# Optimization experiments

Measured on AMD Instinct MI355X. Metric: run time of the kernel, lower is better.

The kernel has to match this reference:

```python
import jax, jax.numpy as jnp
import numpy as np


def setup_inputs() -> dict:
    key = jax.random.key(0)
    ks = jax.random.split(key, 5)
    b, f, h, w, c = 2, 16, 64, 64, 256
    heads, D = 8, 32
    hD = heads * D
    x = jax.random.normal(ks[0], (b, f, h, w, c), dtype=jnp.float32)
    s = 1.0 / np.sqrt(c)
    Wq = jax.random.normal(ks[1], (c, hD), dtype=jnp.float32) * s
    Wk = jax.random.normal(ks[2], (c, hD), dtype=jnp.float32) * s
    Wv = jax.random.normal(ks[3], (c, hD), dtype=jnp.float32) * s
    Wo = jax.random.normal(ks[4], (hD, c), dtype=jnp.float32) * s
    return {"x": x, "Wq": Wq, "Wk": Wk, "Wv": Wv, "Wo": Wo, "heads": heads}


def reference(x, Wq, Wk, Wv, Wo, heads):
    b, f, h, w, c = x.shape
    hD = Wq.shape[1]
    D = hD // heads
    n = h * w
    # fuse batch & frames; 1x1 conv == channel matmul
    xf = x.reshape(b * f, n, c)  # [(bf), n, c]

    def proj(W):
        # [(bf), n, hD] -> [(bf), heads, D, n]
        p = jnp.einsum('bnc,cd->bnd', xf, W)
        return p.reshape(b * f, n, heads, D).transpose(0, 2, 3, 1)

    q = jax.nn.softmax(proj(Wq), axis=-2)  # softmax over D (note: scale is dead code in source)
    k = jax.nn.softmax(proj(Wk), axis=-1)  # softmax over spatial n
    v = proj(Wv)
    context = jnp.einsum('bhdn,bhen->bhde', k, v)      # [(bf), heads, D, D]
    out = jnp.einsum('bhde,bhdn->bhen', context, q)    # [(bf), heads, D, n]
    out = out.transpose(0, 3, 1, 2).reshape(b * f, n, hD)
    out = jnp.einsum('bnd,dc->bnc', out, Wo)
    return out.reshape(b, f, h, w, c)
```

## Files before the change

### kernel.cpp

```cpp
#include <hip/hip_runtime.h>
#include <hip/hip_bf16.h>


typedef __attribute__((ext_vector_type(8))) short bf16x8;
typedef __attribute__((ext_vector_type(4))) float f32x4;

__device__ __forceinline__ unsigned short f2bf(float x) {
  union { float f; unsigned u; } c; c.f = x;
  unsigned r = (c.u + 0x7FFFu + ((c.u >> 16) & 1u)) >> 16;
  return (unsigned short)r;
}

__global__ __launch_bounds__(256) void k0_prep(const float* __restrict__ Wq,
                                               const float* __restrict__ Wk,
                                               const float* __restrict__ Wv,
                                               unsigned short* __restrict__ WqT,
                                               unsigned short* __restrict__ WkvT) {
  int r = blockIdx.x, c = threadIdx.x;
  if (r < 256)      WqT [(r      )*256 + c] = f2bf(Wq[c*256 + r]);
  else if (r < 512) WkvT[(r - 256)*256 + c] = f2bf(Wk[c*256 + (r-256)]);
  else              WkvT[(r - 256)*256 + c] = f2bf(Wv[c*256 + (r-512)]);
}

__global__ __launch_bounds__(512, 2) void k1p(const float* __restrict__ x,
                                              const unsigned short* __restrict__ WkvT,
                                              float* __restrict__ ctxp) {
  __shared__ unsigned short As[2][32*256];
  __shared__ unsigned short slab[512*32];
  int bid = blockIdx.x;
  size_t rowbase = (size_t)bid * 256;
  int tid = threadIdx.x;
  int lane = tid & 63, wid = tid >> 6;
  int cl = lane & 15, rq = (lane >> 4) << 2, fs = lane >> 4;

  bf16x8 bfr[4][8];
#pragma unroll
  for (int nf = 0; nf < 4; ++nf)
#pragma unroll
    for (int kk = 0; kk < 8; ++kk)
      bfr[nf][kk] = *(const bf16x8*)(WkvT + (size_t)(wid*64 + nf*16 + cl)*256 + kk*32 + fs*8);

  f32x4 c2a = {}, c2b = {}, c2c = {}, c2d = {};
  f32x4 c3a = {}, c3b = {};
  bf16x8 bone;
#pragma unroll
  for (int j = 0; j < 8; ++j) bone[j] = (short)0x3F80;

  int ar = tid >> 5, as_ = tid & 31;
  int aw0 = ar*256 + ((as_ ^ (ar & 7)) << 3);
  int aw1 = (16 + ar)*256 + ((as_ ^ (ar & 7)) << 3);
  const float* ap = x + (rowbase + ar)*256 + as_*8;

  float4 pa0 = *(const float4*)ap;
  float4 pa1 = *(const float4*)(ap + 4);
  float4 pa2 = *(const float4*)(ap + 16*256);
  float4 pa3 = *(const float4*)(ap + 16*256 + 4);

  for (int t = 0; t < 8; ++t) {
    unsigned short* Ab = &As[t & 1][0];
    {
      union { ushort4 u4[2]; int4 i4; } pk;
      pk.u4[0].x = f2bf(pa0.x); pk.u4[0].y = f2bf(pa0.y); pk.u4[0].z = f2bf(pa0.z); pk.u4[0].w = f2bf(pa0.w);
      pk.u4[1].x = f2bf(pa1.x); pk.u4[1].y = f2bf(pa1.y); pk.u4[1].z = f2bf(pa1.z); pk.u4[1].w = f2bf(pa1.w);
      *(int4*)(&Ab[aw0]) = pk.i4;
      pk.u4[0].x = f2bf(pa2.x); pk.u4[0].y = f2bf(pa2.y); pk.u4[0].z = f2bf(pa2.z); pk.u4[0].w = f2bf(pa2.w);
      pk.u4[1].x = f2bf(pa3.x); pk.u4[1].y = f2bf(pa3.y); pk.u4[1].z = f2bf(pa3.z); pk.u4[1].w = f2bf(pa3.w);
      *(int4*)(&Ab[aw1]) = pk.i4;
    }
    __syncthreads();
    if (t < 7) {
      const float* apn = ap + (size_t)(t + 1)*32*256;
      pa0 = *(const float4*)apn;
      pa1 = *(const float4*)(apn + 4);
      pa2 = *(const float4*)(apn + 16*256);
      pa3 = *(const float4*)(apn + 16*256 + 4);
    }
    f32x4 acc0[4] = {};
    f32x4 acc1[4] = {};
#pragma unroll
    for (int kk = 0; kk < 8; ++kk) {
      int so = (((kk*4 + fs) ^ (cl & 7)) << 3);
      bf16x8 a0 = *(const bf16x8*)(&Ab[cl*256 + so]);
      bf16x8 a1 = *(const bf16x8*)(&Ab[(16 + cl)*256 + so]);
#pragma unroll
      for (int ni = 0; ni < 4; ++ni) {
        acc0[ni] = __builtin_amdgcn_mfma_f32_16x16x32_bf16(a0, bfr[ni][kk], acc0[ni], 0, 0, 0);
        acc1[ni] = __builtin_amdgcn_mfma_f32_16x16x32_bf16(a1, bfr[ni][kk], acc1[ni], 0, 0, 0);
      }
    }
#pragma unroll
    for (int ni = 0; ni < 4; ++ni) {
      int c = wid*64 + ni*16 + cl;
      int sw = (c ^ (c >> 2)) & 3;
      ushort4 w0, w1;
      if (wid < 4) {
        w0.x = f2bf(__expf(acc0[ni][0])); w0.y = f2bf(__expf(acc0[ni][1]));
        w0.z = f2bf(__expf(acc0[ni][2])); w0.w = f2bf(__expf(acc0[ni][3]));
        w1.x = f2bf(__expf(acc1[ni][0])); w1.y = f2bf(__expf(acc1[ni][1]));
        w1.z = f2bf(__expf(acc1[ni][2])); w1.w = f2bf(__expf(acc1[ni][3]));
      } else {
        w0.x = f2bf(acc0[ni][0]); w0.y = f2bf(acc0[ni][1]);
        w0.z = f2bf(acc0[ni][2]); w0.w = f2bf(acc0[ni][3]);
        w1.x = f2bf(acc1[ni][0]); w1.y = f2bf(acc1[ni][1]);
        w1.z = f2bf(acc1[ni][2]); w1.w = f2bf(acc1[ni][3]);
      }
      *(ushort4*)(&slab[c*32 + (((rq >> 3) ^ sw) << 3) + (rq & 7)]) = w0;
      *(ushort4*)(&slab[c*32 + ((((16 + rq) >> 3) ^ sw) << 3) + (rq & 7)]) = w1;
    }
    __syncthreads();
    {
      int ca0 = wid*32 + cl,        ca1 = wid*32 + 16 + cl;
      int cb0 = 256 + wid*32 + cl,  cb1 = 256 + wid*32 + 16 + cl;
      bf16x8 af0 = *(const bf16x8*)(&slab[ca0*32 + ((fs ^ ((ca0 ^ (ca0 >> 2)) & 3)) << 3)]);
      bf16x8 af1 = *(const bf16x8*)(&slab[ca1*32 + ((fs ^ ((ca1 ^ (ca1 >> 2)) & 3)) << 3)]);
      bf16x8 bv0 = *(const bf16x8*)(&slab[cb0*32 + ((fs ^ ((cb0 ^ (cb0 >> 2)) & 3)) << 3)]);
      bf16x8 bv1 = *(const bf16x8*)(&slab[cb1*32 + ((fs ^ ((cb1 ^ (cb1 >> 2)) & 3)) << 3)]);
      c2a = __builtin_amdgcn_mfma_f32_16x16x32_bf16(af0, bv0, c2a, 0, 0, 0);
      c2b = __builtin_amdgcn_mfma_f32_16x16x32_bf16(af0, bv1, c2b, 0, 0, 0);
      c2c = __builtin_amdgcn_mfma_f32_16x16x32_bf16(af1, bv0, c2c, 0, 0, 0);
      c2d = __builtin_amdgcn_mfma_f32_16x16x32_bf16(af1, bv1, c2d, 0, 0, 0);
      c3a = __builtin_amdgcn_mfma_f32_16x16x32_bf16(af0, bone, c3a, 0, 0, 0);
      c3b = __builtin_amdgcn_mfma_f32_16x16x32_bf16(af1, bone, c3b, 0, 0, 0);
    }
  }
  float* cp = ctxp + ((size_t)bid*8 + wid)*1056;
#pragma unroll
  for (int r = 0; r < 4; ++r) {
    cp[(rq + r)*33 + cl]            = c2a[r];
    cp[(rq + r)*33 + 16 + cl]       = c2b[r];
    cp[(16 + rq + r)*33 + cl]       = c2c[r];
    cp[(16 + rq + r)*33 + 16 + cl]  = c2d[r];
  }
  if (cl == 0) {
#pragma unroll
    for (int r = 0; r < 4; ++r) {
      cp[(rq + r)*33 + 32]      = c3a[r];
      cp[(16 + rq + r)*33 + 32] = c3b[r];
    }
  }
}

__global__ __launch_bounds__(256) void k2b_w2(const float* __restrict__ ctxp,
                                              const float* __restrict__ Wo,
                                              unsigned short* __restrict__ W2t) {
  __shared__ float clds[32*33];
  int bid = blockIdx.x;
  int h = bid & 7, bfi = bid >> 3;
  int tid = threadIdx.x;
  for (int i = tid; i < 1056; i += 256) {
    float s = 0.f;
#pragma unroll
    for (int p = 0; p < 16; ++p)
      s += ctxp[((size_t)(bfi*16 + p)*8 + h)*1056 + i];
    clds[i] = s;
  }
  __syncthreads();
  float acc[32] = {};
#pragma unroll 4
  for (int e = 0; e < 32; ++e) {
    float w = Wo[(size_t)(h*32 + e)*256 + tid];
#pragma unroll
    for (int d = 0; d < 32; ++d) acc[d] += clds[d*33 + e] * w;
  }
  unsigned short* o = W2t + ((size_t)bfi*256 + tid)*256 + h*32;
#pragma unroll
  for (int d = 0; d < 32; ++d) o[d] = f2bf(acc[d] / clds[d*33 + 32]);
}

__global__ __launch_bounds__(512, 2) void k3p(const float* __restrict__ x,
                                              const unsigned short* __restrict__ WqT,
                                              const unsigned short* __restrict__ W2t,
                                              float* __restrict__ out) {
  __shared__ unsigned short As[2][32*256];
  __shared__ unsigned short Qs[2][32*256];
  int bid = blockIdx.x;
  size_t rowbase = (size_t)bid * 256;
  int bfi = bid >> 4;
  int tid = threadIdx.x;
  int lane = tid & 63, wid = tid >> 6;
  int cl = lane & 15, rq = (lane >> 4) << 2, fs = lane >> 4;

  bf16x8 bq[2][8], bw[2][8];
#pragma unroll
  for (int nf = 0; nf < 2; ++nf)
#pragma unroll
    for (int kk = 0; kk < 8; ++kk) {
      bq[nf][kk] = *(const bf16x8*)(WqT + (size_t)(wid*32 + nf*16 + cl)*256 + kk*32 + fs*8);
      bw[nf][kk] = *(const bf16x8*)(W2t + ((size_t)bfi*256 + wid*32 + nf*16 + cl)*256 + kk*32 + fs*8);
    }

  int ar = tid >> 5, as_ = tid & 31;
  int aw0 = ar*256 + ((as_ ^ (ar & 7)) << 3);
  int aw1 = (16 + ar)*256 + ((as_ ^ (ar & 7)) << 3);
  const float* ap = x + (rowbase + ar)*256 + as_*8;

  float4 pa0 = *(const float4*)ap;
  float4 pa1 = *(const float4*)(ap + 4);
  float4 pa2 = *(const float4*)(ap + 16*256);
  float4 pa3 = *(const float4*)(ap + 16*256 + 4);

  for (int t = 0; t < 8; ++t) {
    unsigned short* Ab = &As[t & 1][0];
    unsigned short* Qb = &Qs[t & 1][0];
    {
      union { ushort4 u4[2]; int4 i4; } pk;
      pk.u4[0].x = f2bf(pa0.x); pk.u4[0].y = f2bf(pa0.y); pk.u4[0].z = f2bf(pa0.z); pk.u4[0].w = f2bf(pa0.w);
      pk.u4[1].x = f2bf(pa1.x); pk.u4[1].y = f2bf(pa1.y); pk.u4[1].z = f2bf(pa1.z); pk.u4[1].w = f2bf(pa1.w);
      *(int4*)(&Ab[aw0]) = pk.i4;
      pk.u4[0].x = f2bf(pa2.x); pk.u4[0].y = f2bf(pa2.y); pk.u4[0].z = f2bf(pa2.z); pk.u4[0].w = f2bf(pa2.w);
      pk.u4[1].x = f2bf(pa3.x); pk.u4[1].y = f2bf(pa3.y); pk.u4[1].z = f2bf(pa3.z); pk.u4[1].w = f2bf(pa3.w);
      *(int4*)(&Ab[aw1]) = pk.i4;
    }
    __syncthreads();
    if (t < 7) {
      const float* apn = ap + (size_t)(t + 1)*32*256;
      pa0 = *(const float4*)apn;
      pa1 = *(const float4*)(apn + 4);
      pa2 = *(const float4*)(apn + 16*256);
      pa3 = *(const float4*)(apn + 16*256 + 4);
    }
    f32x4 ql[2][2] = {};
#pragma unroll
    for (int kk = 0; kk < 8; ++kk) {
      int so = (((kk*4 + fs) ^ (cl & 7)) << 3);
      bf16x8 a0 = *(const bf16x8*)(&Ab[cl*256 + so]);
      bf16x8 a1 = *(const bf16x8*)(&Ab[(16 + cl)*256 + so]);
#pragma unroll
      for (int nf = 0; nf < 2; ++nf) {
        ql[0][nf] = __builtin_amdgcn_mfma_f32_16x16x32_bf16(a0, bq[nf][kk], ql[0][nf], 0, 0, 0);
        ql[1][nf] = __builtin_amdgcn_mfma_f32_16x16x32_bf16(a1, bq[nf][kk], ql[1][nf], 0, 0, 0);
      }
    }
#pragma unroll
    for (int mf = 0; mf < 2; ++mf) {
#pragma unroll
      for (int r = 0; r < 4; ++r) {
        float e0 = __expf(ql[mf][0][r]);
        float e1 = __expf(ql[mf][1][r]);
        float s = e0 + e1;
        s += __shfl_xor(s, 1); s += __shfl_xor(s, 2);
        s += __shfl_xor(s, 4); s += __shfl_xor(s, 8);
        float inv = 1.0f / s;
        int row = mf*16 + rq + r;
        int c0 = wid*32 + cl;
        int c1 = wid*32 + 16 + cl;
        Qb[row*256 + (((c0 >> 3) ^ (row & 7)) << 3) + (c0 & 7)] = f2bf(e0 * inv);
        Qb[row*256 + (((c1 >> 3) ^ (row & 7)) << 3) + (c1 & 7)] = f2bf(e1 * inv);
      }
    }
    __syncthreads();
    f32x4 oa[2][2] = {};
#pragma unroll
    for (int kk = 0; kk < 8; ++kk) {
      int so = (((kk*4 + fs) ^ (cl & 7)) << 3);
      bf16x8 a0 = *(const bf16x8*)(&Qb[cl*256 + so]);
      bf16x8 a1 = *(const bf16x8*)(&Qb[(16 + cl)*256 + so]);
#pragma unroll
      for (int nf = 0; nf < 2; ++nf) {
        oa[0][nf] = __builtin_amdgcn_mfma_f32_16x16x32_bf16(a0, bw[nf][kk], oa[0][nf], 0, 0, 0);
        oa[1][nf] = __builtin_amdgcn_mfma_f32_16x16x32_bf16(a1, bw[nf][kk], oa[1][nf], 0, 0, 0);
      }
    }
    size_t ob = rowbase + (size_t)t*32;
#pragma unroll
    for (int mf = 0; mf < 2; ++mf)
#pragma unroll
      for (int nf = 0; nf < 2; ++nf)
#pragma unroll
        for (int r = 0; r < 4; ++r)
          out[(ob + mf*16 + rq + r)*256 + wid*32 + nf*16 + cl] = oa[mf][nf][r];
  }
}

extern "C" void kernel_launch(void* const* d_in, const int* in_sizes, int n_in,
                              void* d_out, int out_size, void* d_ws, size_t ws_size,
                              hipStream_t stream) {
  const float* x  = (const float*)d_in[0];
  const float* Wq = (const float*)d_in[1];
  const float* Wk = (const float*)d_in[2];
  const float* Wv = (const float*)d_in[3];
  const float* Wo = (const float*)d_in[4];
  float* out = (float*)d_out;

  unsigned short* WkvT = (unsigned short*)d_ws;
  unsigned short* WqT  = WkvT + 131072;
  unsigned short* W2t  = WqT  + 65536;
  float*          ctxp = (float*)(W2t + 2097152);

  k0_prep <<<768,  256, 0, stream>>>(Wq, Wk, Wv, WqT, WkvT);
  k1p     <<<512,  512, 0, stream>>>(x, WkvT, ctxp);
  k2b_w2  <<<256,  256, 0, stream>>>(ctxp, Wo, W2t);
  k3p     <<<512,  512, 0, stream>>>(x, WqT, W2t, out);
}
```

Before: 159.2 us.

## Software-pipeline k3 projection/softmax with output GEMM and transpose MFMA operands

Restructures the final fused kernel so that the Q projection and softmax for the next 32-row tile run in the same barrier interval as the output GEMM for the current tile, which halves the __syncthreads per iteration. MFMA operands are swapped so each lane holds four consecutive rows. That lets the softmax reduce with two cross-lane shuffles instead of four, pack Q to LDS as ushort4, and write outputs as float4 rather than scalar stores. The float-to-bf16 conversion is also switched to the HIP intrinsic. In exchange the kernel carries more registers (qpk, the prefetch registers) and a longer prologue and epilogue.

```diff
diff --git a/kernel.cpp b/kernel.cpp
--- a/kernel.cpp
+++ b/kernel.cpp
@@ -6,9 +6,8 @@
 typedef __attribute__((ext_vector_type(4))) float f32x4;
 
 __device__ __forceinline__ unsigned short f2bf(float x) {
-  union { float f; unsigned u; } c; c.f = x;
-  unsigned r = (c.u + 0x7FFFu + ((c.u >> 16) & 1u)) >> 16;
-  return (unsigned short)r;
+  __hip_bfloat16 h = __float2bfloat16(x);
+  union { __hip_bfloat16 b; unsigned short u; } c; c.b = h; return c.u;
 }
 
 __global__ __launch_bounds__(256) void k0_prep(const float* __restrict__ Wq,
@@ -167,7 +166,7 @@
   for (int d = 0; d < 32; ++d) o[d] = f2bf(acc[d] / clds[d*33 + 32]);
 }
 
-__global__ __launch_bounds__(512, 2) void k3p(const float* __restrict__ x,
+__global__ __launch_bounds__(512, 2) void k3s(const float* __restrict__ x,
                                               const unsigned short* __restrict__ WqT,
                                               const unsigned short* __restrict__ W2t,
                                               float* __restrict__ out) {
@@ -194,15 +193,59 @@
   int aw1 = (16 + ar)*256 + ((as_ ^ (ar & 7)) << 3);
   const float* ap = x + (rowbase + ar)*256 + as_*8;
 
+  int qslotbase = wid*4 + (rq >> 3);
+  ushort4 qpk[2][2];
+
   float4 pa0 = *(const float4*)ap;
   float4 pa1 = *(const float4*)(ap + 4);
   float4 pa2 = *(const float4*)(ap + 16*256);
   float4 pa3 = *(const float4*)(ap + 16*256 + 4);
-
-  for (int t = 0; t < 8; ++t) {
-    unsigned short* Ab = &As[t & 1][0];
-    unsigned short* Qb = &Qs[t & 1][0];
-    {
+  {
+    unsigned short* Ab = &As[0][0];
+    union { ushort4 u4[2]; int4 i4; } pk;
+    pk.u4[0].x = f2bf(pa0.x); pk.u4[0].y = f2bf(pa0.y); pk.u4[0].z = f2bf(pa0.z); pk.u4[0].w = f2bf(pa0.w);
+    pk.u4[1].x = f2bf(pa1.x); pk.u4[1].y = f2bf(pa1.y); pk.u4[1].z = f2bf(pa1.z); pk.u4[1].w = f2bf(pa1.w);
+    *(int4*)(&Ab[aw0]) = pk.i4;
+    pk.u4[0].x = f2bf(pa2.x); pk.u4[0].y = f2bf(pa2.y); pk.u4[0].z = f2bf(pa2.z); pk.u4[0].w = f2bf(pa2.w);
+    pk.u4[1].x = f2bf(pa3.x); pk.u4[1].y = f2bf(pa3.y); pk.u4[1].z = f2bf(pa3.z); pk.u4[1].w = f2bf(pa3.w);
+    *(int4*)(&Ab[aw1]) = pk.i4;
+  }
+  {
+    const float* apn = ap + 32*256;
+    pa0 = *(const float4*)apn;
+    pa1 = *(const float4*)(apn + 4);
+    pa2 = *(const float4*)(apn + 16*256);
+    pa3 = *(const float4*)(apn + 16*256 + 4);
+  }
+  __syncthreads();
+  {
+    unsigned short* Ab = &As[0][0];
+    f32x4 ql[2][2] = {};
+#pragma unroll
+    for (int kk = 0; kk < 8; ++kk) {
+      int so = (((kk*4 + fs) ^ (cl & 7)) << 3);
+      bf16x8 a0 = *(const bf16x8*)(&Ab[cl*256 + so]);
+      bf16x8 a1 = *(const bf16x8*)(&Ab[(16 + cl)*256 + so]);
+#pragma unroll
+      for (int nf = 0; nf < 2; ++nf) {
+        ql[0][nf] = __builtin_amdgcn_mfma_f32_16x16x32_bf16(bq[nf][kk], a0, ql[0][nf], 0, 0, 0);
+        ql[1][nf] = __builtin_amdgcn_mfma_f32_16x16x32_bf16(bq[nf][kk], a1, ql[1][nf], 0, 0, 0);
+      }
+    }
+#pragma unroll
+    for (int m = 0; m < 2; ++m) {
+      float e0[4], e1[4]; float s8 = 0.f;
+#pragma unroll
+      for (int r = 0; r < 4; ++r) { e0[r] = __expf(ql[m][0][r]); e1[r] = __expf(ql[m][1][r]); s8 += e0[r] + e1[r]; }
+      float s = s8; s += __shfl_xor(s, 16); s += __shfl_xor(s, 32);
+      float inv = 1.0f / s;
+      qpk[m][0].x = f2bf(e0[0]*inv); qpk[m][0].y = f2bf(e0[1]*inv); qpk[m][0].z = f2bf(e0[2]*inv); qpk[m][0].w = f2bf(e0[3]*inv);
+      qpk[m][1].x = f2bf(e1[0]*inv); qpk[m][1].y = f2bf(e1[1]*inv); qpk[m][1].z = f2bf(e1[2]*inv); qpk[m][1].w = f2bf(e1[3]*inv);
+    }
+  }
+  for (int t = 0; t < 7; ++t) {
+    {
+      unsigned short* Ab = &As[(t + 1) & 1][0];
       union { ushort4 u4[2]; int4 i4; } pk;
       pk.u4[0].x = f2bf(pa0.x); pk.u4[0].y = f2bf(pa0.y); pk.u4[0].z = f2bf(pa0.z); pk.u4[0].w = f2bf(pa0.w);
       pk.u4[1].x = f2bf(pa1.x); pk.u4[1].y = f2bf(pa1.y); pk.u4[1].z = f2bf(pa1.z); pk.u4[1].w = f2bf(pa1.w);
@@ -211,64 +254,104 @@
       pk.u4[1].x = f2bf(pa3.x); pk.u4[1].y = f2bf(pa3.y); pk.u4[1].z = f2bf(pa3.z); pk.u4[1].w = f2bf(pa3.w);
       *(int4*)(&Ab[aw1]) = pk.i4;
     }
-    __syncthreads();
-    if (t < 7) {
-      const float* apn = ap + (size_t)(t + 1)*32*256;
+    {
+      unsigned short* Qb = &Qs[t & 1][0];
+#pragma unroll
+      for (int m = 0; m < 2; ++m) {
+        int row = m*16 + cl;
+#pragma unroll
+        for (int nf = 0; nf < 2; ++nf) {
+          int slot = qslotbase + nf*2;
+          *(ushort4*)(&Qb[row*256 + ((slot ^ (row & 7)) << 3) + (rq & 4)]) = qpk[m][nf];
+        }
+      }
+    }
+    if (t < 6) {
+      const float* apn = ap + (size_t)(t + 2)*32*256;
       pa0 = *(const float4*)apn;
       pa1 = *(const float4*)(apn + 4);
       pa2 = *(const float4*)(apn + 16*256);
       pa3 = *(const float4*)(apn + 16*256 + 4);
     }
-    f32x4 ql[2][2] = {};
+    __syncthreads();
+    f32x4 oa[2][2] = {};
+    {
+      unsigned short* Qb = &Qs[t & 1][0];
+#pragma unroll
+      for (int kk = 0; kk < 8; ++kk) {
+        int so = (((kk*4 + fs) ^ (cl & 7)) << 3);
+        bf16x8 q0 = *(const bf16x8*)(&Qb[cl*256 + so]);
+        bf16x8 q1 = *(const bf16x8*)(&Qb[(16 + cl)*256 + so]);
+#pragma unroll
+        for (int nf = 0; nf < 2; ++nf) {
+          oa[0][nf] = __builtin_amdgcn_mfma_f32_16x16x32_bf16(bw[nf][kk], q0, oa[0][nf], 0, 0, 0);
+          oa[1][nf] = __builtin_amdgcn_mfma_f32_16x16x32_bf16(bw[nf][kk], q1, oa[1][nf], 0, 0, 0);
+        }
+      }
+    }
+    {
+      unsigned short* Ab = &As[(t + 1) & 1][0];
+      f32x4 ql[2][2] = {};
+#pragma unroll
+      for (int kk = 0; kk < 8; ++kk) {
+        int so = (((kk*4 + fs) ^ (cl & 7)) << 3);
+        bf16x8 a0 = *(const bf16x8*)(&Ab[cl*256 + so]);
+        bf16x8 a1 = *(const bf16x8*)(&Ab[(16 + cl)*256 + so]);
+#pragma unroll
+        for (int nf = 0; nf < 2; ++nf) {
+          ql[0][nf] = __builtin_amdgcn_mfma_f32_16x16x32_bf16(bq[nf][kk], a0, ql[0][nf], 0, 0, 0);
+          ql[1][nf] = __builtin_amdgcn_mfma_f32_16x16x32_bf16(bq[nf][kk], a1, ql[1][nf], 0, 0, 0);
+        }
+      }
+#pragma unroll
+      for (int m = 0; m < 2; ++m) {
+        float e0[4], e1[4]; float s8 = 0.f;
+#pragma unroll
+        for (int r = 0; r < 4; ++r) { e0[r] = __expf(ql[m][0][r]); e1[r] = __expf(ql[m][1][r]); s8 += e0[r] + e1[r]; }
+        float s = s8; s += __shfl_xor(s, 16); s += __shfl_xor(s, 32);
+        float inv = 1.0f / s;
+        qpk[m][0].x = f2bf(e0[0]*inv); qpk[m][0].y = f2bf(e0[1]*inv); qpk[m][0].z = f2bf(e0[2]*inv); qpk[m][0].w = f2bf(e0[3]*inv);
+        qpk[m][1].x = f2bf(e1[0]*inv); qpk[m][1].y = f2bf(e1[1]*inv); qpk[m][1].z = f2bf(e1[2]*inv); qpk[m][1].w = f2bf(e1[3]*inv);
+      }
+    }
+#pragma unroll
+    for (int m = 0; m < 2; ++m)
+#pragma unroll
+      for (int nf = 0; nf < 2; ++nf)
+        *(f32x4*)(&out[(rowbase + (size_t)t*32 + m*16 + cl)*256 + wid*32 + nf*16 + rq]) = oa[m][nf];
+  }
+  {
+    unsigned short* Qb = &Qs[1][0];
+#pragma unroll
+    for (int m = 0; m < 2; ++m) {
+      int row = m*16 + cl;
+#pragma unroll
+      for (int nf = 0; nf < 2; ++nf) {
+        int slot = qslotbase + nf*2;
+        *(ushort4*)(&Qb[row*256 + ((slot ^ (row & 7)) << 3) + (rq & 4)]) = qpk[m][nf];
+      }
+    }
+  }
+  __syncthreads();
+  {
+    unsigned short* Qb = &Qs[1][0];
+    f32x4 oa[2][2] = {};
 #pragma unroll
     for (int kk = 0; kk < 8; ++kk) {
       int so = (((kk*4 + fs) ^ (cl & 7)) << 3);
-      bf16x8 a0 = *(const bf16x8*)(&Ab[cl*256 + so]);
-      bf16x8 a1 = *(const bf16x8*)(&Ab[(16 + cl)*256 + so]);
+      bf16x8 q0 = *(const bf16x8*)(&Qb[cl*256 + so]);
+      bf16x8 q1 = *(const bf16x8*)(&Qb[(16 + cl)*256 + so]);
 #pragma unroll
       for (int nf = 0; nf < 2; ++nf) {
-        ql[0][nf] = __builtin_amdgcn_mfma_f32_16x16x32_bf16(a0, bq[nf][kk], ql[0][nf], 0, 0, 0);
-        ql[1][nf] = __builtin_amdgcn_mfma_f32_16x16x32_bf16(a1, bq[nf][kk], ql[1][nf], 0, 0, 0);
-      }
-    }
-#pragma unroll
-    for (int mf = 0; mf < 2; ++mf) {
-#pragma unroll
-      for (int r = 0; r < 4; ++r) {
-        float e0 = __expf(ql[mf][0][r]);
-        float e1 = __expf(ql[mf][1][r]);
-        float s = e0 + e1;
-        s += __shfl_xor(s, 1); s += __shfl_xor(s, 2);
-        s += __shfl_xor(s, 4); s += __shfl_xor(s, 8);
-        float inv = 1.0f / s;
-        int row = mf*16 + rq + r;
-        int c0 = wid*32 + cl;
-        int c1 = wid*32 + 16 + cl;
-        Qb[row*256 + (((c0 >> 3) ^ (row & 7)) << 3) + (c0 & 7)] = f2bf(e0 * inv);
-        Qb[row*256 + (((c1 >> 3) ^ (row & 7)) << 3) + (c1 & 7)] = f2bf(e1 * inv);
-      }
-    }
-    __syncthreads();
-    f32x4 oa[2][2] = {};
-#pragma unroll
-    for (int kk = 0; kk < 8; ++kk) {
-      int so = (((kk*4 + fs) ^ (cl & 7)) << 3);
-      bf16x8 a0 = *(const bf16x8*)(&Qb[cl*256 + so]);
-      bf16x8 a1 = *(const bf16x8*)(&Qb[(16 + cl)*256 + so]);
-#pragma unroll
-      for (int nf = 0; nf < 2; ++nf) {
-        oa[0][nf] = __builtin_amdgcn_mfma_f32_16x16x32_bf16(a0, bw[nf][kk], oa[0][nf], 0, 0, 0);
-        oa[1][nf] = __builtin_amdgcn_mfma_f32_16x16x32_bf16(a1, bw[nf][kk], oa[1][nf], 0, 0, 0);
-      }
-    }
-    size_t ob = rowbase + (size_t)t*32;
-#pragma unroll
-    for (int mf = 0; mf < 2; ++mf)
+        oa[0][nf] = __builtin_amdgcn_mfma_f32_16x16x32_bf16(bw[nf][kk], q0, oa[0][nf], 0, 0, 0);
+        oa[1][nf] = __builtin_amdgcn_mfma_f32_16x16x32_bf16(bw[nf][kk], q1, oa[1][nf], 0, 0, 0);
+      }
+    }
+#pragma unroll
+    for (int m = 0; m < 2; ++m)
 #pragma unroll
       for (int nf = 0; nf < 2; ++nf)
-#pragma unroll
-        for (int r = 0; r < 4; ++r)
-          out[(ob + mf*16 + rq + r)*256 + wid*32 + nf*16 + cl] = oa[mf][nf][r];
+        *(f32x4*)(&out[(rowbase + (size_t)7*32 + m*16 + cl)*256 + wid*32 + nf*16 + rq]) = oa[m][nf];
   }
 }
 
@@ -290,5 +373,5 @@
   k0_prep <<<768,  256, 0, stream>>>(Wq, Wk, Wv, WqT, WkvT);
   k1p     <<<512,  512, 0, stream>>>(x, WkvT, ctxp);
   k2b_w2  <<<256,  256, 0, stream>>>(ctxp, Wo, W2t);
-  k3p     <<<512,  512, 0, stream>>>(x, WqT, W2t, out);
-}
+  k3s     <<<512,  512, 0, stream>>>(x, WqT, W2t, out);
+}
```

Result: faster. 141.9 us (-10.8%).
